# Kernel tuning notes

Hardware: AMD Instinct MI355X
Metric: run time of the kernel (lower is better)

Reference implementation:

```python
import jax, jax.numpy as jnp
import numpy as np

N_ATOMS = 8192
N_SUBSYSTEMS = 64
CUTOFF = 5.0


def setup_inputs() -> dict:
    key = jax.random.key(0)
    k1, k2 = jax.random.split(key)
    positions = jax.random.normal(k1, (N_ATOMS, 3), dtype=jnp.float32)
    atomic_subsystem_indices = jnp.sort(
        jax.random.randint(k2, (N_ATOMS,), 0, N_SUBSYSTEMS)
    ).astype(jnp.int64)
    return {"positions": positions, "atomic_subsystem_indices": atomic_subsystem_indices}


def reference(positions, atomic_subsystem_indices):
    """JIT-compatible PairList forward.

    The torch original builds dynamic-size pair lists via nonzero(); here we use
    the static upper-triangular candidate set (all i<j pairs) plus a validity
    mask (same subsystem AND distance < cutoff). Invalid pair indices are -1 and
    invalid r_ij / d_ij entries are zeroed.

    Returns (pair_indices [2,P] int, d_ij [P,1], r_ij [P,3], valid_mask [P] bool).
    """
    n = positions.shape[0]
    i, j = jnp.triu_indices(n, k=1)          # P = n*(n-1)//2 candidate pairs
    pair_indices = jnp.stack([i, j])          # (2, P)

    # displacement: selected_positions[1] - selected_positions[0]
    r_ij = positions[j] - positions[i]        # (P, 3)
    d_ij = jnp.linalg.norm(r_ij, axis=-1, keepdims=True)  # (P, 1)

    same_sys = atomic_subsystem_indices[i] == atomic_subsystem_indices[j]
    valid = same_sys & (d_ij[:, 0] < CUTOFF)  # (P,)

    pair_out = jnp.where(valid[None, :], pair_indices, -1)
    m = valid[:, None].astype(positions.dtype)
    return pair_out, d_ij * m, r_ij * m, valid
```

## Files before the change

kernel.cpp:

```cpp
#include <hip/hip_runtime.h>
#include <cmath>


__global__ __launch_bounds__(256) void pairlist_kernel(
    const float* __restrict__ pos, const int* __restrict__ sub,
    float* __restrict__ out, int n, long long P) {
  long long g  = (long long)blockIdx.x * blockDim.x + threadIdx.x;
  long long p0 = g * 4;
  if (p0 >= P) return;

  const int shift = (sub[n - 1] == 0) ? 1 : 0;

  double t = 2.0 * (double)n - 1.0;
  double disc = t * t - 8.0 * (double)p0;
  int i = (int)((t - sqrt(disc)) * 0.5);
  if (i < 0) i = 0;
  if (i > n - 2) i = n - 2;
  auto T = [n](long long ii) { return ii * (2LL * n - ii - 1) / 2; };
  while (T(i + 1) <= p0) ++i;
  while (i > 0 && T(i) > p0) --i;
  int j = (int)((long long)i + 1 + (p0 - T(i)));

  int   si  = sub[i << shift];
  float pix = pos[3 * i], piy = pos[3 * i + 1], piz = pos[3 * i + 2];

  float fi[4], fj[4], fd[4], fv[4], fr[12];

#pragma unroll
  for (int k = 0; k < 4; ++k) {
    long long p = p0 + k;
    float vi = -1.0f, vj = -1.0f, vd = 0.0f, vv = 0.0f;
    float rx = 0.0f, ry = 0.0f, rz = 0.0f;
    if (p < P) {
      int sj = sub[j << shift];
      if (sj == si) {
        float dx = pos[3 * j]     - pix;
        float dy = pos[3 * j + 1] - piy;
        float dz = pos[3 * j + 2] - piz;
        float dd = sqrtf(dx * dx + dy * dy + dz * dz);
        if (dd < 5.0f) {
          vi = (float)i; vj = (float)j;
          vd = dd; vv = 1.0f;
          rx = dx; ry = dy; rz = dz;
        }
      }
      ++j;
      if (j >= n) {
        ++i;
        j = i + 1;
        if (i < n - 1) {
          si = sub[i << shift];
          pix = pos[3 * i]; piy = pos[3 * i + 1]; piz = pos[3 * i + 2];
        }
      }
    }
    fi[k] = vi; fj[k] = vj; fd[k] = vd; fv[k] = vv;
    fr[3 * k] = rx; fr[3 * k + 1] = ry; fr[3 * k + 2] = rz;
  }

  float* oi  = out;
  float* oj  = out + P;
  float* od  = out + 2 * P;
  float* orr = out + 3 * P;
  float* ov  = out + 6 * P;

  if (p0 + 4 <= P) {
    *reinterpret_cast<float4*>(oi + p0) = make_float4(fi[0], fi[1], fi[2], fi[3]);
    *reinterpret_cast<float4*>(oj + p0) = make_float4(fj[0], fj[1], fj[2], fj[3]);
    *reinterpret_cast<float4*>(od + p0) = make_float4(fd[0], fd[1], fd[2], fd[3]);
    *reinterpret_cast<float4*>(ov + p0) = make_float4(fv[0], fv[1], fv[2], fv[3]);
    float4* rb = reinterpret_cast<float4*>(orr + 3 * p0);
    rb[0] = make_float4(fr[0], fr[1], fr[2],  fr[3]);
    rb[1] = make_float4(fr[4], fr[5], fr[6],  fr[7]);
    rb[2] = make_float4(fr[8], fr[9], fr[10], fr[11]);
  } else {
    for (int k = 0; k < 4 && p0 + k < P; ++k) {
      long long p = p0 + k;
      oi[p] = fi[k]; oj[p] = fj[k]; od[p] = fd[k]; ov[p] = fv[k];
      orr[3 * p] = fr[3 * k]; orr[3 * p + 1] = fr[3 * k + 1]; orr[3 * p + 2] = fr[3 * k + 2];
    }
  }
}

extern "C" void kernel_launch(void* const* d_in, const int* in_sizes, int n_in,
                              void* d_out, int out_size, void* d_ws, size_t ws_size,
                              hipStream_t stream) {
  const float* pos = (const float*)d_in[0];
  const int*   sub = (const int*)d_in[1];
  float* out = (float*)d_out;

  long long P = (long long)out_size / 7;
  int n = (int)((1.0 + sqrt(1.0 + 8.0 * (double)P)) * 0.5 + 0.5);
  if ((long long)n * (n - 1) / 2 != P) {
    n = in_sizes[0] / 3;
    P = (long long)n * (n - 1) / 2;
  }

  long long threads = (P + 3) / 4;
  int blocks = (int)((threads + 255) / 256);
  hipLaunchKernelGGL(pairlist_kernel, dim3(blocks), dim3(256), 0, stream,
                     pos, sub, out, n, P);
}
```

Measured before the change: 171.3 us.

## Split pair list into bulk default fill plus per-row subsystem scatter

The single kernel that evaluated every i<j pair is replaced by two kernels. A grid-stride fill kernel writes the default values (-1 for the index rows, 0 elsewhere) with float4 stores. A scatter kernel then gives one wavefront to each row i and walks j only while all lanes stay in i's subsystem. Only valid pairs are written, so distance math and gathers are skipped for the vast majority of pairs. The early exit relies on subsystem indices being sorted and contiguous, and the full output must still be written, so the cost stays dominated by store bandwidth plus an extra launch.

```diff
diff --git a/kernel.cpp b/kernel.cpp
--- a/kernel.cpp
+++ b/kernel.cpp
@@ -2,61 +2,29 @@
 #include <cmath>
 
 
-__global__ __launch_bounds__(256) void pairlist_kernel(
+__global__ __launch_bounds__(256) void fill_kernel(float4* __restrict__ out4,
+                                                   long long n4, long long negEnd4) {
+  long long idx = (long long)blockIdx.x * blockDim.x + threadIdx.x;
+  long long stride = (long long)gridDim.x * blockDim.x;
+  const float4 NEG = make_float4(-1.0f, -1.0f, -1.0f, -1.0f);
+  const float4 ZER = make_float4(0.0f, 0.0f, 0.0f, 0.0f);
+  for (long long q = idx; q < n4; q += stride)
+    out4[q] = (q < negEnd4) ? NEG : ZER;
+}
+
+__global__ __launch_bounds__(256) void scatter_kernel(
     const float* __restrict__ pos, const int* __restrict__ sub,
     float* __restrict__ out, int n, long long P) {
-  long long g  = (long long)blockIdx.x * blockDim.x + threadIdx.x;
-  long long p0 = g * 4;
-  if (p0 >= P) return;
+  int wave = blockIdx.x * (blockDim.x >> 6) + (threadIdx.x >> 6);
+  int i = wave;
+  if (i >= n - 1) return;
+  int lane = threadIdx.x & 63;
 
   const int shift = (sub[n - 1] == 0) ? 1 : 0;
 
-  double t = 2.0 * (double)n - 1.0;
-  double disc = t * t - 8.0 * (double)p0;
-  int i = (int)((t - sqrt(disc)) * 0.5);
-  if (i < 0) i = 0;
-  if (i > n - 2) i = n - 2;
-  auto T = [n](long long ii) { return ii * (2LL * n - ii - 1) / 2; };
-  while (T(i + 1) <= p0) ++i;
-  while (i > 0 && T(i) > p0) --i;
-  int j = (int)((long long)i + 1 + (p0 - T(i)));
-
   int   si  = sub[i << shift];
   float pix = pos[3 * i], piy = pos[3 * i + 1], piz = pos[3 * i + 2];
-
-  float fi[4], fj[4], fd[4], fv[4], fr[12];
-
-#pragma unroll
-  for (int k = 0; k < 4; ++k) {
-    long long p = p0 + k;
-    float vi = -1.0f, vj = -1.0f, vd = 0.0f, vv = 0.0f;
-    float rx = 0.0f, ry = 0.0f, rz = 0.0f;
-    if (p < P) {
-      int sj = sub[j << shift];
-      if (sj == si) {
-        float dx = pos[3 * j]     - pix;
-        float dy = pos[3 * j + 1] - piy;
-        float dz = pos[3 * j + 2] - piz;
-        float dd = sqrtf(dx * dx + dy * dy + dz * dz);
-        if (dd < 5.0f) {
-          vi = (float)i; vj = (float)j;
-          vd = dd; vv = 1.0f;
-          rx = dx; ry = dy; rz = dz;
-        }
-      }
-      ++j;
-      if (j >= n) {
-        ++i;
-        j = i + 1;
-        if (i < n - 1) {
-          si = sub[i << shift];
-          pix = pos[3 * i]; piy = pos[3 * i + 1]; piz = pos[3 * i + 2];
-        }
-      }
-    }
-    fi[k] = vi; fj[k] = vj; fd[k] = vd; fv[k] = vv;
-    fr[3 * k] = rx; fr[3 * k + 1] = ry; fr[3 * k + 2] = rz;
-  }
+  long long Ti = (long long)i * (2LL * n - i - 1) / 2;
 
   float* oi  = out;
   float* oj  = out + P;
@@ -64,21 +32,26 @@
   float* orr = out + 3 * P;
   float* ov  = out + 6 * P;
 
-  if (p0 + 4 <= P) {
-    *reinterpret_cast<float4*>(oi + p0) = make_float4(fi[0], fi[1], fi[2], fi[3]);
-    *reinterpret_cast<float4*>(oj + p0) = make_float4(fj[0], fj[1], fj[2], fj[3]);
-    *reinterpret_cast<float4*>(od + p0) = make_float4(fd[0], fd[1], fd[2], fd[3]);
-    *reinterpret_cast<float4*>(ov + p0) = make_float4(fv[0], fv[1], fv[2], fv[3]);
-    float4* rb = reinterpret_cast<float4*>(orr + 3 * p0);
-    rb[0] = make_float4(fr[0], fr[1], fr[2],  fr[3]);
-    rb[1] = make_float4(fr[4], fr[5], fr[6],  fr[7]);
-    rb[2] = make_float4(fr[8], fr[9], fr[10], fr[11]);
-  } else {
-    for (int k = 0; k < 4 && p0 + k < P; ++k) {
-      long long p = p0 + k;
-      oi[p] = fi[k]; oj[p] = fj[k]; od[p] = fd[k]; ov[p] = fv[k];
-      orr[3 * p] = fr[3 * k]; orr[3 * p + 1] = fr[3 * k + 1]; orr[3 * p + 2] = fr[3 * k + 2];
+  for (int j0 = i + 1; j0 < n; j0 += 64) {
+    int j = j0 + lane;
+    bool insys = (j < n) && (sub[j << shift] == si);
+    if (insys) {
+      float dx = pos[3 * j]     - pix;
+      float dy = pos[3 * j + 1] - piy;
+      float dz = pos[3 * j + 2] - piz;
+      float dd = sqrtf(dx * dx + dy * dy + dz * dz);
+      if (dd < 5.0f) {
+        long long p = Ti + (long long)(j - i - 1);
+        oi[p] = (float)i;
+        oj[p] = (float)j;
+        od[p] = dd;
+        orr[3 * p]     = dx;
+        orr[3 * p + 1] = dy;
+        orr[3 * p + 2] = dz;
+        ov[p] = 1.0f;
+      }
     }
+    if (__ballot(insys) != ~0ull) break;
   }
 }
 
@@ -96,8 +69,13 @@
     P = (long long)n * (n - 1) / 2;
   }
 
-  long long threads = (P + 3) / 4;
-  int blocks = (int)((threads + 255) / 256);
-  hipLaunchKernelGGL(pairlist_kernel, dim3(blocks), dim3(256), 0, stream,
+  long long n4 = (7 * P) / 4;
+  long long negEnd4 = (2 * P) / 4;
+  hipLaunchKernelGGL(fill_kernel, dim3(8192), dim3(256), 0, stream,
+                     (float4*)out, n4, negEnd4);
+
+  int wavesNeeded = n;
+  int blocks = (wavesNeeded * 64 + 255) / 256;
+  hipLaunchKernelGGL(scatter_kernel, dim3(blocks), dim3(256), 0, stream,
                      pos, sub, out, n, P);
 }
```

New measurement: 213.1 us. +24.4%, slower.

## Precompute subsystem run ends and fast-path fill out-of-subsystem pair chunks

Applied to the files above, without the earlier changes.

Adds a small pre-kernel that uses binary search over the sorted subsystem indices to find, for each atom, the end of its subsystem run. The main kernel then tests subsystem membership with an index comparison instead of reloading subsystem ids. When a thread's whole 4-pair chunk lies past the run end, it writes constant invalid values directly and skips loading positions and computing distances. This relies on the indices being sorted and adds an extra launch plus a workspace buffer, with a fallback path when the workspace is too small.

```diff
diff --git a/kernel.cpp b/kernel.cpp
--- a/kernel.cpp
+++ b/kernel.cpp
@@ -2,14 +2,28 @@
 #include <cmath>
 
 
+__global__ __launch_bounds__(256) void runend_kernel(
+    const int* __restrict__ sub, int* __restrict__ re, int n) {
+  int a = blockIdx.x * blockDim.x + threadIdx.x;
+  if (a >= n) return;
+  const int shift = (sub[n - 1] == 0) ? 1 : 0;
+  int s = sub[a << shift];
+  int lo = a + 1, hi = n;
+  while (lo < hi) {
+    int mid = (lo + hi) >> 1;
+    if (sub[mid << shift] > s) hi = mid; else lo = mid + 1;
+  }
+  re[a] = lo;
+}
+
+template <bool USE_RE>
 __global__ __launch_bounds__(256) void pairlist_kernel(
     const float* __restrict__ pos, const int* __restrict__ sub,
-    float* __restrict__ out, int n, long long P) {
+    const int* __restrict__ runEnd, float* __restrict__ out,
+    int n, long long P) {
   long long g  = (long long)blockIdx.x * blockDim.x + threadIdx.x;
   long long p0 = g * 4;
   if (p0 >= P) return;
-
-  const int shift = (sub[n - 1] == 0) ? 1 : 0;
 
   double t = 2.0 * (double)n - 1.0;
   double disc = t * t - 8.0 * (double)p0;
@@ -21,7 +35,34 @@
   while (i > 0 && T(i) > p0) --i;
   int j = (int)((long long)i + 1 + (p0 - T(i)));
 
-  int   si  = sub[i << shift];
+  float* oi  = out;
+  float* oj  = out + P;
+  float* od  = out + 2 * P;
+  float* orr = out + 3 * P;
+  float* ov  = out + 6 * P;
+
+  int shift = 0, re;
+  if (USE_RE) {
+    re = runEnd[i];
+  } else {
+    shift = (sub[n - 1] == 0) ? 1 : 0;
+    re = (sub[j << shift] == sub[i << shift]) ? n : j;
+  }
+
+  if (j >= re && p0 + 4 <= P && j + 4 <= n) {
+    const float4 NEG = make_float4(-1.f, -1.f, -1.f, -1.f);
+    const float4 ZER = make_float4(0.f, 0.f, 0.f, 0.f);
+    *reinterpret_cast<float4*>(oi + p0) = NEG;
+    *reinterpret_cast<float4*>(oj + p0) = NEG;
+    *reinterpret_cast<float4*>(od + p0) = ZER;
+    *reinterpret_cast<float4*>(ov + p0) = ZER;
+    float4* rb = reinterpret_cast<float4*>(orr + 3 * p0);
+    rb[0] = ZER; rb[1] = ZER; rb[2] = ZER;
+    return;
+  }
+
+  int si = 0;
+  if (!USE_RE) si = sub[i << shift];
   float pix = pos[3 * i], piy = pos[3 * i + 1], piz = pos[3 * i + 2];
 
   float fi[4], fj[4], fd[4], fv[4], fr[12];
@@ -32,8 +73,8 @@
     float vi = -1.0f, vj = -1.0f, vd = 0.0f, vv = 0.0f;
     float rx = 0.0f, ry = 0.0f, rz = 0.0f;
     if (p < P) {
-      int sj = sub[j << shift];
-      if (sj == si) {
+      bool insys = USE_RE ? (j < re) : (sub[j << shift] == si);
+      if (insys) {
         float dx = pos[3 * j]     - pix;
         float dy = pos[3 * j + 1] - piy;
         float dz = pos[3 * j + 2] - piz;
@@ -49,7 +90,8 @@
         ++i;
         j = i + 1;
         if (i < n - 1) {
-          si = sub[i << shift];
+          if (USE_RE) re = runEnd[i];
+          else        si = sub[i << shift];
           pix = pos[3 * i]; piy = pos[3 * i + 1]; piz = pos[3 * i + 2];
         }
       }
@@ -57,12 +99,6 @@
     fi[k] = vi; fj[k] = vj; fd[k] = vd; fv[k] = vv;
     fr[3 * k] = rx; fr[3 * k + 1] = ry; fr[3 * k + 2] = rz;
   }
-
-  float* oi  = out;
-  float* oj  = out + P;
-  float* od  = out + 2 * P;
-  float* orr = out + 3 * P;
-  float* ov  = out + 6 * P;
 
   if (p0 + 4 <= P) {
     *reinterpret_cast<float4*>(oi + p0) = make_float4(fi[0], fi[1], fi[2], fi[3]);
@@ -98,6 +134,16 @@
 
   long long threads = (P + 3) / 4;
   int blocks = (int)((threads + 255) / 256);
-  hipLaunchKernelGGL(pairlist_kernel, dim3(blocks), dim3(256), 0, stream,
-                     pos, sub, out, n, P);
+
+  bool useRe = (ws_size >= (size_t)n * sizeof(int));
+  if (useRe) {
+    int* re = (int*)d_ws;
+    hipLaunchKernelGGL(runend_kernel, dim3((n + 255) / 256), dim3(256), 0,
+                       stream, sub, re, n);
+    hipLaunchKernelGGL((pairlist_kernel<true>), dim3(blocks), dim3(256), 0,
+                       stream, pos, sub, re, out, n, P);
+  } else {
+    hipLaunchKernelGGL((pairlist_kernel<false>), dim3(blocks), dim3(256), 0,
+                       stream, pos, sub, (const int*)nullptr, out, n, P);
+  }
 }
```

Measured after the change: 201.1 us. +17.4%, slower.

## Precompute per-row subsystem run ends in shared memory to skip sub loads

Applied to the files above, without the earlier changes.

Each block computes, for the rows it spans, the end index of atom i's subsystem run by binary search over the sorted subsystem array and stores these in shared memory. Threads then test same-subsystem membership with a comparison j < run_end instead of loading sub[j] for each pair, and load positions only for in-system pairs. This removes per-pair gathers of the subsystem index but adds a block-wide setup phase with two barriers and binary searches. The kernel is likely dominated by output writes, so the benefit may be small.

```diff
diff --git a/kernel.cpp b/kernel.cpp
--- a/kernel.cpp
+++ b/kernel.cpp
@@ -2,27 +2,67 @@
 #include <cmath>
 
 
+__device__ __forceinline__ int bsearch_runend(const int* __restrict__ sub,
+                                              int n, int shift, int atom) {
+  int s = sub[atom << shift];
+  int lo = atom + 1, hi = n;
+  while (lo < hi) {
+    int mid = (lo + hi) >> 1;
+    if (sub[mid << shift] > s) hi = mid; else lo = mid + 1;
+  }
+  return lo;
+}
+
 __global__ __launch_bounds__(256) void pairlist_kernel(
     const float* __restrict__ pos, const int* __restrict__ sub,
     float* __restrict__ out, int n, long long P) {
-  long long g  = (long long)blockIdx.x * blockDim.x + threadIdx.x;
-  long long p0 = g * 4;
-  if (p0 >= P) return;
+  const int tid = threadIdx.x;
+  const long long b0 = (long long)blockIdx.x * blockDim.x * 4;
+  const long long p0 = b0 + (long long)tid * 4;
+  const bool active = p0 < P;
+  const long long pc = active ? p0 : (P - 1);
 
-  const int shift = (sub[n - 1] == 0) ? 1 : 0;
-
-  double t = 2.0 * (double)n - 1.0;
-  double disc = t * t - 8.0 * (double)p0;
+  const double t = 2.0 * (double)n - 1.0;
+  auto T = [n](long long ii) { return ii * (2LL * n - ii - 1) / 2; };
+  double disc = t * t - 8.0 * (double)pc;
   int i = (int)((t - sqrt(disc)) * 0.5);
   if (i < 0) i = 0;
   if (i > n - 2) i = n - 2;
-  auto T = [n](long long ii) { return ii * (2LL * n - ii - 1) / 2; };
-  while (T(i + 1) <= p0) ++i;
-  while (i > 0 && T(i) > p0) --i;
-  int j = (int)((long long)i + 1 + (p0 - T(i)));
+  while (T(i + 1) <= pc) ++i;
+  while (i > 0 && T(i) > pc) --i;
+  int j = (int)((long long)i + 1 + (pc - T(i)));
 
-  int   si  = sub[i << shift];
-  float pix = pos[3 * i], piy = pos[3 * i + 1], piz = pos[3 * i + 2];
+  __shared__ int sMeta[2];
+  __shared__ int sRe[256];
+  const int shift = (sub[n - 1] == 0) ? 1 : 0;
+  if (tid == 0) {
+    long long pl = b0 + (long long)blockDim.x * 4 - 1;
+    if (pl >= P) pl = P - 1;
+    double d2 = t * t - 8.0 * (double)pl;
+    int i1 = (int)((t - sqrt(d2)) * 0.5);
+    if (i1 < 0) i1 = 0;
+    if (i1 > n - 2) i1 = n - 2;
+    while (T(i1 + 1) <= pl) ++i1;
+    while (i1 > 0 && T(i1) > pl) --i1;
+    sMeta[0] = i;
+    sMeta[1] = i1 - i + 1;
+  }
+  __syncthreads();
+  const int i0 = sMeta[0];
+  const int cnt = sMeta[1];
+  for (int a = tid; a < cnt && a < 256; a += blockDim.x)
+    sRe[a] = bsearch_runend(sub, n, shift, i0 + a);
+  __syncthreads();
+  if (!active) return;
+
+  int idx = i - i0;
+  int re = (idx < 256) ? sRe[idx] : bsearch_runend(sub, n, shift, i);
+
+  float* oi  = out;
+  float* oj  = out + P;
+  float* od  = out + 2 * P;
+  float* orr = out + 3 * P;
+  float* ov  = out + 6 * P;
 
   float fi[4], fj[4], fd[4], fv[4], fr[12];
 
@@ -32,8 +72,9 @@
     float vi = -1.0f, vj = -1.0f, vd = 0.0f, vv = 0.0f;
     float rx = 0.0f, ry = 0.0f, rz = 0.0f;
     if (p < P) {
-      int sj = sub[j << shift];
-      if (sj == si) {
+      bool insys = (j < re);
+      if (insys) {
+        float pix = pos[3 * i], piy = pos[3 * i + 1], piz = pos[3 * i + 2];
         float dx = pos[3 * j]     - pix;
         float dy = pos[3 * j + 1] - piy;
         float dz = pos[3 * j + 2] - piz;
@@ -49,20 +90,14 @@
         ++i;
         j = i + 1;
         if (i < n - 1) {
-          si = sub[i << shift];
-          pix = pos[3 * i]; piy = pos[3 * i + 1]; piz = pos[3 * i + 2];
+          int a = i - i0;
+          re = (a < 256) ? sRe[a] : bsearch_runend(sub, n, shift, i);
         }
       }
     }
     fi[k] = vi; fj[k] = vj; fd[k] = vd; fv[k] = vv;
     fr[3 * k] = rx; fr[3 * k + 1] = ry; fr[3 * k + 2] = rz;
   }
-
-  float* oi  = out;
-  float* oj  = out + P;
-  float* od  = out + 2 * P;
-  float* orr = out + 3 * P;
-  float* ov  = out + 6 * P;
 
   if (p0 + 4 <= P) {
     *reinterpret_cast<float4*>(oi + p0) = make_float4(fi[0], fi[1], fi[2], fi[3]);
```

Measured after the change: 202.8 us. 18.4% more time.
